# Kernel optimization log

Measured on AMD Instinct MI355X. Metric: run time of the kernel, lower is better.

Reference implementation:

```python
import jax, jax.numpy as jnp
import numpy as np

B = 2_000_000  # number of 6x6 stiffness matrices

def setup_inputs() -> dict:
    key = jax.random.key(0)
    C = jax.random.normal(key, (B, 6, 6), dtype=jnp.float32)
    return {"C": C}

def reference(C) -> jnp.ndarray:
    # matrix_power_4: C^4 via two repeated squarings, batched over leading dim
    C2 = jnp.matmul(C, C)   # [B,6,6]
    return jnp.matmul(C2, C2)
```

## Files before the change

### kernel.cpp

```cpp
#include <hip/hip_runtime.h>


#define MPB 256

#define GLOBAL_AS __attribute__((address_space(1)))
#define LDS_AS    __attribute__((address_space(3)))

__global__ __launch_bounds__(256, 4) void matpow4_kernel(
    const float* __restrict__ C, float* __restrict__ out, int B)
{
    __shared__ float4 lds4[MPB * 9];

    const int tid = threadIdx.x;
    const long long mbase = (long long)blockIdx.x * MPB;
    const int nm = (int)min((long long)MPB, (long long)B - mbase);
    const int nf4 = nm * 9;

    const float4* __restrict__ src = reinterpret_cast<const float4*>(C) + mbase * 9;

#pragma unroll
    for (int k = 0; k < 9; ++k) {
        int f = k * MPB + tid;
        if (f < nf4) {
            __builtin_amdgcn_global_load_lds(
                (const GLOBAL_AS void*)(src + f),
                (LDS_AS void*)(&lds4[f]),
                16, 0, 0);
        }
    }
    __syncthreads();

    if (tid < nm) {
        float a[36], b[36];
#pragma unroll
        for (int j = 0; j < 9; ++j) {
            float4 v = lds4[tid * 9 + j];
            a[4 * j + 0] = v.x;
            a[4 * j + 1] = v.y;
            a[4 * j + 2] = v.z;
            a[4 * j + 3] = v.w;
        }

#pragma unroll
        for (int i = 0; i < 6; ++i) {
#pragma unroll
            for (int j = 0; j < 6; ++j) {
                float s = a[i * 6 + 0] * a[0 * 6 + j];
#pragma unroll
                for (int k = 1; k < 6; ++k)
                    s = fmaf(a[i * 6 + k], a[k * 6 + j], s);
                b[i * 6 + j] = s;
            }
        }
#pragma unroll
        for (int i = 0; i < 6; ++i) {
#pragma unroll
            for (int j = 0; j < 6; ++j) {
                float s = b[i * 6 + 0] * b[0 * 6 + j];
#pragma unroll
                for (int k = 1; k < 6; ++k)
                    s = fmaf(b[i * 6 + k], b[k * 6 + j], s);
                a[i * 6 + j] = s;
            }
        }

#pragma unroll
        for (int j = 0; j < 9; ++j) {
            float4 v;
            v.x = a[4 * j + 0];
            v.y = a[4 * j + 1];
            v.z = a[4 * j + 2];
            v.w = a[4 * j + 3];
            lds4[tid * 9 + j] = v;
        }
    }
    __syncthreads();

    float4* __restrict__ dst = reinterpret_cast<float4*>(out) + mbase * 9;
#pragma unroll
    for (int k = 0; k < 9; ++k) {
        int f = k * MPB + tid;
        if (f < nf4) {
            dst[f] = lds4[f];
        }
    }
}

extern "C" void kernel_launch(void* const* d_in, const int* in_sizes, int n_in,
                              void* d_out, int out_size, void* d_ws, size_t ws_size,
                              hipStream_t stream)
{
    const float* C = (const float*)d_in[0];
    float* out = (float*)d_out;
    int B = in_sizes[0] / 36;

    int grid = (B + MPB - 1) / MPB;
    matpow4_kernel<<<grid, MPB, 0, stream>>>(C, out, B);
}
```

Measured before the change: 110.1 us.

## Use persistent double-buffered blocks to overlap async LDS loads with compute

Replaces the one-block-per-256-matrices launch with a fixed grid of 512 persistent blocks. Each block walks chunks in a grid-stride loop and double-buffers them in LDS, prefetching the next chunk through global_load_lds while the current one is squared twice and stored. Synchronisation uses hand-placed vmcnt/lgkmcnt waits and raw s_barrier. The aim is to hide global-load latency and cut launch and tail costs. In exchange LDS use per block doubles, occupancy drops to 2 blocks per CU, and correctness depends on the manual waitcnt accounting, including the stores that also count against vmcnt.

Measured after the change: 111.8 us. Within noise of the previous version (+1.6%).

```diff
diff --git a/kernel.cpp b/kernel.cpp
--- a/kernel.cpp
+++ b/kernel.cpp
@@ -2,86 +2,154 @@
 
 
 #define MPB 256
+#define NB  512
 
 #define GLOBAL_AS __attribute__((address_space(1)))
 #define LDS_AS    __attribute__((address_space(3)))
 
-__global__ __launch_bounds__(256, 4) void matpow4_kernel(
-    const float* __restrict__ C, float* __restrict__ out, int B)
+#define WAITV0()  asm volatile("s_waitcnt vmcnt(0)" ::: "memory")
+#define WAITV9()  asm volatile("s_waitcnt vmcnt(9)" ::: "memory")
+#define WAITV18() asm volatile("s_waitcnt vmcnt(18)" ::: "memory")
+#define WAITL()   asm volatile("s_waitcnt lgkmcnt(0)" ::: "memory")
+#define BAR()     asm volatile("s_barrier" ::: "memory")
+
+__device__ __forceinline__ void pow4_regs(float a[36])
 {
-    __shared__ float4 lds4[MPB * 9];
+    float b[36];
+#pragma unroll
+    for (int i = 0; i < 6; ++i)
+#pragma unroll
+        for (int j = 0; j < 6; ++j) {
+            float s = a[i * 6 + 0] * a[0 * 6 + j];
+#pragma unroll
+            for (int k = 1; k < 6; ++k)
+                s = fmaf(a[i * 6 + k], a[k * 6 + j], s);
+            b[i * 6 + j] = s;
+        }
+#pragma unroll
+    for (int i = 0; i < 6; ++i)
+#pragma unroll
+        for (int j = 0; j < 6; ++j) {
+            float s = b[i * 6 + 0] * b[0 * 6 + j];
+#pragma unroll
+            for (int k = 1; k < 6; ++k)
+                s = fmaf(b[i * 6 + k], b[k * 6 + j], s);
+            a[i * 6 + j] = s;
+        }
+}
+
+__global__ __launch_bounds__(256, 2) void matpow4_pipe(
+    const float* __restrict__ C, float* __restrict__ out, int nchunk, int B)
+{
+    __shared__ float4 lds4[2][MPB * 9];
 
     const int tid = threadIdx.x;
-    const long long mbase = (long long)blockIdx.x * MPB;
-    const int nm = (int)min((long long)MPB, (long long)B - mbase);
-    const int nf4 = nm * 9;
+    const int bid = blockIdx.x;
 
-    const float4* __restrict__ src = reinterpret_cast<const float4*>(C) + mbase * 9;
+    const float4* __restrict__ srcAll = reinterpret_cast<const float4*>(C);
+    float4* __restrict__ dstAll = reinterpret_cast<float4*>(out);
 
+    const int n = (bid < nchunk) ? (nchunk - bid + NB - 1) / NB : 0;
+
+    if (n > 0) {
+        {
+            const float4* src = srcAll + (size_t)bid * MPB * 9;
 #pragma unroll
-    for (int k = 0; k < 9; ++k) {
-        int f = k * MPB + tid;
-        if (f < nf4) {
-            __builtin_amdgcn_global_load_lds(
-                (const GLOBAL_AS void*)(src + f),
-                (LDS_AS void*)(&lds4[f]),
-                16, 0, 0);
-        }
-    }
-    __syncthreads();
-
-    if (tid < nm) {
-        float a[36], b[36];
-#pragma unroll
-        for (int j = 0; j < 9; ++j) {
-            float4 v = lds4[tid * 9 + j];
-            a[4 * j + 0] = v.x;
-            a[4 * j + 1] = v.y;
-            a[4 * j + 2] = v.z;
-            a[4 * j + 3] = v.w;
-        }
-
-#pragma unroll
-        for (int i = 0; i < 6; ++i) {
-#pragma unroll
-            for (int j = 0; j < 6; ++j) {
-                float s = a[i * 6 + 0] * a[0 * 6 + j];
-#pragma unroll
-                for (int k = 1; k < 6; ++k)
-                    s = fmaf(a[i * 6 + k], a[k * 6 + j], s);
-                b[i * 6 + j] = s;
-            }
-        }
-#pragma unroll
-        for (int i = 0; i < 6; ++i) {
-#pragma unroll
-            for (int j = 0; j < 6; ++j) {
-                float s = b[i * 6 + 0] * b[0 * 6 + j];
-#pragma unroll
-                for (int k = 1; k < 6; ++k)
-                    s = fmaf(b[i * 6 + k], b[k * 6 + j], s);
-                a[i * 6 + j] = s;
+            for (int k = 0; k < 9; ++k) {
+                int f = k * MPB + tid;
+                __builtin_amdgcn_global_load_lds(
+                    (const GLOBAL_AS void*)(src + f),
+                    (LDS_AS void*)(&lds4[0][f]), 16, 0, 0);
             }
         }
 
+        for (int t = 0; t < n; ++t) {
+            const int cur = t & 1;
+            const bool pf = (t + 1 < n);
+
+            if (pf) {
+                const int c = bid + (t + 1) * NB;
+                const float4* src = srcAll + (size_t)c * MPB * 9;
 #pragma unroll
-        for (int j = 0; j < 9; ++j) {
-            float4 v;
-            v.x = a[4 * j + 0];
-            v.y = a[4 * j + 1];
-            v.z = a[4 * j + 2];
-            v.w = a[4 * j + 3];
-            lds4[tid * 9 + j] = v;
+                for (int k = 0; k < 9; ++k) {
+                    int f = k * MPB + tid;
+                    __builtin_amdgcn_global_load_lds(
+                        (const GLOBAL_AS void*)(src + f),
+                        (LDS_AS void*)(&lds4[cur ^ 1][f]), 16, 0, 0);
+                }
+            }
+
+            if (t == 0) {
+                if (pf) { WAITV9(); } else { WAITV0(); }
+            } else if (pf) {
+                WAITV18();
+            } else {
+                WAITV9();
+            }
+            BAR();
+
+            {
+                float a[36];
+#pragma unroll
+                for (int j = 0; j < 9; ++j) {
+                    float4 v = lds4[cur][tid * 9 + j];
+                    a[4 * j + 0] = v.x;
+                    a[4 * j + 1] = v.y;
+                    a[4 * j + 2] = v.z;
+                    a[4 * j + 3] = v.w;
+                }
+                pow4_regs(a);
+#pragma unroll
+                for (int j = 0; j < 9; ++j) {
+                    float4 v;
+                    v.x = a[4 * j + 0];
+                    v.y = a[4 * j + 1];
+                    v.z = a[4 * j + 2];
+                    v.w = a[4 * j + 3];
+                    lds4[cur][tid * 9 + j] = v;
+                }
+            }
+            WAITL();
+            BAR();
+
+            {
+                const int c = bid + t * NB;
+                float4* dst = dstAll + (size_t)c * MPB * 9;
+#pragma unroll
+                for (int k = 0; k < 9; ++k) {
+                    int f = k * MPB + tid;
+                    dst[f] = lds4[cur][f];
+                }
+            }
+            WAITL();
+            BAR();
         }
     }
-    __syncthreads();
 
-    float4* __restrict__ dst = reinterpret_cast<float4*>(out) + mbase * 9;
+    if (bid == 0) {
+        int idx = nchunk * MPB + tid;
+        if (idx < B) {
+            const float4* src = srcAll + (size_t)idx * 9;
+            float a[36];
 #pragma unroll
-    for (int k = 0; k < 9; ++k) {
-        int f = k * MPB + tid;
-        if (f < nf4) {
-            dst[f] = lds4[f];
+            for (int j = 0; j < 9; ++j) {
+                float4 v = src[j];
+                a[4 * j + 0] = v.x;
+                a[4 * j + 1] = v.y;
+                a[4 * j + 2] = v.z;
+                a[4 * j + 3] = v.w;
+            }
+            pow4_regs(a);
+            float4* dst = dstAll + (size_t)idx * 9;
+#pragma unroll
+            for (int j = 0; j < 9; ++j) {
+                float4 v;
+                v.x = a[4 * j + 0];
+                v.y = a[4 * j + 1];
+                v.z = a[4 * j + 2];
+                v.w = a[4 * j + 3];
+                dst[j] = v;
+            }
         }
     }
 }
@@ -94,6 +162,6 @@
     float* out = (float*)d_out;
     int B = in_sizes[0] / 36;
 
-    int grid = (B + MPB - 1) / MPB;
-    matpow4_kernel<<<grid, MPB, 0, stream>>>(C, out, B);
+    int nchunk = B / MPB;
+    matpow4_pipe<<<NB, MPB, 0, stream>>>(C, out, nchunk, B);
 }
```

## Convert matpow4 to persistent grid-stride kernel with nontemporal stores

Applied to the files above, without the earlier changes.

Replaces the one-block-per-chunk launch with a fixed grid of 1024 persistent blocks. Each block loops over 256-matrix chunks and loads them into LDS with an async global-to-LDS copy carrying a cache-policy hint. Output goes out through nontemporal stores, and full chunks drop their bounds checks, with a remainder path handled by the last block. The aim is to cut block launch and tail overhead and to keep streaming output from polluting the cache. In exchange there is no overlap between chunks, since each iteration serializes load, compute and store behind barriers, and the fixed grid size may underfill or unbalance the CUs.

After: 109.9 us. About the same (-0.2%).

```diff
diff --git a/kernel.cpp b/kernel.cpp
--- a/kernel.cpp
+++ b/kernel.cpp
@@ -2,86 +2,119 @@
 
 
 #define MPB 256
+#define NB  1024
 
 #define GLOBAL_AS __attribute__((address_space(1)))
 #define LDS_AS    __attribute__((address_space(3)))
 
-__global__ __launch_bounds__(256, 4) void matpow4_kernel(
-    const float* __restrict__ C, float* __restrict__ out, int B)
+typedef float f32x4 __attribute__((ext_vector_type(4)));
+
+__device__ __forceinline__ void pow4_regs(float a[36])
 {
-    __shared__ float4 lds4[MPB * 9];
+    float b[36];
+#pragma unroll
+    for (int i = 0; i < 6; ++i)
+#pragma unroll
+        for (int j = 0; j < 6; ++j) {
+            float s = a[i * 6 + 0] * a[0 * 6 + j];
+#pragma unroll
+            for (int k = 1; k < 6; ++k)
+                s = fmaf(a[i * 6 + k], a[k * 6 + j], s);
+            b[i * 6 + j] = s;
+        }
+#pragma unroll
+    for (int i = 0; i < 6; ++i)
+#pragma unroll
+        for (int j = 0; j < 6; ++j) {
+            float s = b[i * 6 + 0] * b[0 * 6 + j];
+#pragma unroll
+            for (int k = 1; k < 6; ++k)
+                s = fmaf(b[i * 6 + k], b[k * 6 + j], s);
+            a[i * 6 + j] = s;
+        }
+}
+
+__global__ __launch_bounds__(256, 4) void matpow4_persist(
+    const float* __restrict__ C, float* __restrict__ out, int nchunk, int B)
+{
+    __shared__ f32x4 lds4[MPB * 9];
 
     const int tid = threadIdx.x;
-    const long long mbase = (long long)blockIdx.x * MPB;
-    const int nm = (int)min((long long)MPB, (long long)B - mbase);
-    const int nf4 = nm * 9;
+    const int bid = blockIdx.x;
 
-    const float4* __restrict__ src = reinterpret_cast<const float4*>(C) + mbase * 9;
+    const f32x4* __restrict__ srcAll = reinterpret_cast<const f32x4*>(C);
+    f32x4* __restrict__ dstAll = reinterpret_cast<f32x4*>(out);
+
+    for (int c = bid; c < nchunk; c += NB) {
+        const f32x4* src = srcAll + (size_t)c * (MPB * 9);
 
 #pragma unroll
-    for (int k = 0; k < 9; ++k) {
-        int f = k * MPB + tid;
-        if (f < nf4) {
+        for (int k = 0; k < 9; ++k) {
+            int f = k * MPB + tid;
             __builtin_amdgcn_global_load_lds(
                 (const GLOBAL_AS void*)(src + f),
-                (LDS_AS void*)(&lds4[f]),
-                16, 0, 0);
+                (LDS_AS void*)(&lds4[f]), 16, 0,  2);
         }
-    }
-    __syncthreads();
+        __syncthreads();
 
-    if (tid < nm) {
-        float a[36], b[36];
+        {
+            float a[36];
 #pragma unroll
-        for (int j = 0; j < 9; ++j) {
-            float4 v = lds4[tid * 9 + j];
-            a[4 * j + 0] = v.x;
-            a[4 * j + 1] = v.y;
-            a[4 * j + 2] = v.z;
-            a[4 * j + 3] = v.w;
+            for (int j = 0; j < 9; ++j) {
+                f32x4 v = lds4[tid * 9 + j];
+                a[4 * j + 0] = v.x;
+                a[4 * j + 1] = v.y;
+                a[4 * j + 2] = v.z;
+                a[4 * j + 3] = v.w;
+            }
+            pow4_regs(a);
+#pragma unroll
+            for (int j = 0; j < 9; ++j) {
+                f32x4 v;
+                v.x = a[4 * j + 0];
+                v.y = a[4 * j + 1];
+                v.z = a[4 * j + 2];
+                v.w = a[4 * j + 3];
+                lds4[tid * 9 + j] = v;
+            }
+        }
+        __syncthreads();
+
+#pragma unroll
+        for (int k = 0; k < 9; ++k) {
+            int f = k * MPB + tid;
+            f32x4 v = lds4[f];
+            __builtin_nontemporal_store(v, dstAll + (size_t)c * (MPB * 9) + f);
         }
 
+        asm volatile("s_waitcnt lgkmcnt(0)" ::: "memory");
+        asm volatile("s_barrier" ::: "memory");
+    }
+
+    if (bid == NB - 1) {
+        int idx = nchunk * MPB + tid;
+        if (idx < B) {
+            const f32x4* src = srcAll + (size_t)idx * 9;
+            float a[36];
 #pragma unroll
-        for (int i = 0; i < 6; ++i) {
+            for (int j = 0; j < 9; ++j) {
+                f32x4 v = src[j];
+                a[4 * j + 0] = v.x;
+                a[4 * j + 1] = v.y;
+                a[4 * j + 2] = v.z;
+                a[4 * j + 3] = v.w;
+            }
+            pow4_regs(a);
+            f32x4* dst = dstAll + (size_t)idx * 9;
 #pragma unroll
-            for (int j = 0; j < 6; ++j) {
-                float s = a[i * 6 + 0] * a[0 * 6 + j];
-#pragma unroll
-                for (int k = 1; k < 6; ++k)
-                    s = fmaf(a[i * 6 + k], a[k * 6 + j], s);
-                b[i * 6 + j] = s;
+            for (int j = 0; j < 9; ++j) {
+                f32x4 v;
+                v.x = a[4 * j + 0];
+                v.y = a[4 * j + 1];
+                v.z = a[4 * j + 2];
+                v.w = a[4 * j + 3];
+                dst[j] = v;
             }
-        }
-#pragma unroll
-        for (int i = 0; i < 6; ++i) {
-#pragma unroll
-            for (int j = 0; j < 6; ++j) {
-                float s = b[i * 6 + 0] * b[0 * 6 + j];
-#pragma unroll
-                for (int k = 1; k < 6; ++k)
-                    s = fmaf(b[i * 6 + k], b[k * 6 + j], s);
-                a[i * 6 + j] = s;
-            }
-        }
-
-#pragma unroll
-        for (int j = 0; j < 9; ++j) {
-            float4 v;
-            v.x = a[4 * j + 0];
-            v.y = a[4 * j + 1];
-            v.z = a[4 * j + 2];
-            v.w = a[4 * j + 3];
-            lds4[tid * 9 + j] = v;
-        }
-    }
-    __syncthreads();
-
-    float4* __restrict__ dst = reinterpret_cast<float4*>(out) + mbase * 9;
-#pragma unroll
-    for (int k = 0; k < 9; ++k) {
-        int f = k * MPB + tid;
-        if (f < nf4) {
-            dst[f] = lds4[f];
         }
     }
 }
@@ -94,6 +127,6 @@
     float* out = (float*)d_out;
     int B = in_sizes[0] / 36;
 
-    int grid = (B + MPB - 1) / MPB;
-    matpow4_kernel<<<grid, MPB, 0, stream>>>(C, out, B);
+    int nchunk = B / MPB;
+    matpow4_persist<<<NB, MPB, 0, stream>>>(C, out, nchunk, B);
 }
```
